# Performance work log

Measured on AMD Instinct MI355X. Metric: run time of the kernel, lower is better.

## Reference

```python
import jax, jax.numpy as jnp
import numpy as np
import math

D_MODEL = 1024
NUM_HEADS = 16
D_KEY = D_MODEL // NUM_HEADS  # 64, used only for the softmax scale
B, S = 4, 2048


def setup_inputs() -> dict:
    key = jax.random.key(0)
    ks = jax.random.split(key, 7)
    scale = 1.0 / math.sqrt(D_MODEL)
    x = jax.random.normal(ks[0], (B, S, D_MODEL), dtype=jnp.float32)
    # torch.nn.Linear params: weight [out, in], bias [out]
    Wq = jax.random.normal(ks[1], (D_MODEL, D_MODEL), dtype=jnp.float32) * scale
    bq = jax.random.normal(ks[2], (D_MODEL,), dtype=jnp.float32) * scale
    Wk = jax.random.normal(ks[3], (D_MODEL, D_MODEL), dtype=jnp.float32) * scale
    bk = jax.random.normal(ks[4], (D_MODEL,), dtype=jnp.float32) * scale
    Wv = jax.random.normal(ks[5], (D_MODEL, D_MODEL), dtype=jnp.float32) * scale
    bv = jax.random.normal(ks[6], (D_MODEL,), dtype=jnp.float32) * scale
    return {"x": x, "Wq": Wq, "bq": bq, "Wk": Wk, "bk": bk, "Wv": Wv, "bv": bv}


def reference(x, Wq, bq, Wk, bk, Wv, bv):
    # Q, K, V projections (torch Linear: x @ W.T + b)
    Q = jnp.einsum('bsd,ed->bse', x, Wq) + bq  # [B,S,D]
    K = jnp.einsum('bsd,ed->bse', x, Wk) + bk
    V = jnp.einsum('bsd,ed->bse', x, Wv) + bv
    inv_sqrt_dk = 1.0 / math.sqrt(D_KEY)
    # full-width attention (no head split, as in the source forward)
    scores = jnp.einsum('bqd,bkd->bqk', Q, K) * inv_sqrt_dk  # [B,S,S]
    weights = jax.nn.softmax(scores, axis=-1)
    return jnp.einsum('bqk,bkd->bqd', weights, V)  # [B,S,D]
```

## Files before the change

kernel.cpp:

```cpp
#include <hip/hip_runtime.h>
#include <stdint.h>

#define S_LEN 2048
#define DMODEL 1024
#define NBATCH 4
#define MROWS (NBATCH * S_LEN)

typedef __bf16 bf16x8 __attribute__((ext_vector_type(8)));
typedef float f32x4 __attribute__((ext_vector_type(4)));

__device__ __forceinline__ unsigned short f2bf(float f) {
  unsigned int x = __builtin_bit_cast(unsigned int, f);
  x += 0x7FFFu + ((x >> 16) & 1u);
  return (unsigned short)(x >> 16);
}

template <int N>
__device__ __forceinline__ void waitvm() {
  static_assert(N <= 8, "vmcnt range");
  if constexpr (N < 0) {}
  else if constexpr (N == 0) asm volatile("s_waitcnt vmcnt(0)" ::: "memory");
  else if constexpr (N == 1) asm volatile("s_waitcnt vmcnt(1)" ::: "memory");
  else if constexpr (N == 2) asm volatile("s_waitcnt vmcnt(2)" ::: "memory");
  else if constexpr (N == 3) asm volatile("s_waitcnt vmcnt(3)" ::: "memory");
  else if constexpr (N == 4) asm volatile("s_waitcnt vmcnt(4)" ::: "memory");
  else if constexpr (N == 5) asm volatile("s_waitcnt vmcnt(5)" ::: "memory");
  else if constexpr (N == 6) asm volatile("s_waitcnt vmcnt(6)" ::: "memory");
  else if constexpr (N == 7) asm volatile("s_waitcnt vmcnt(7)" ::: "memory");
  else asm volatile("s_waitcnt vmcnt(8)" ::: "memory");
}
#define BARRIER() do { __builtin_amdgcn_s_barrier(); asm volatile("" ::: "memory"); } while (0)
#define LGKM0() do { asm volatile("s_waitcnt lgkmcnt(0)" ::: "memory"); \
                     __builtin_amdgcn_sched_barrier(0); } while (0)

__global__ void prep_all_kernel(const float* __restrict__ x, const float* __restrict__ Wq,
                                const float* __restrict__ Wk, const float* __restrict__ Wv,
                                const float* __restrict__ bq, const float* __restrict__ bk,
                                ushort4* __restrict__ xb, ushort4* __restrict__ Wqkb,
                                ushort4* __restrict__ Wvb, float4* __restrict__ bqk) {
  const int NX = MROWS * DMODEL / 4;
  const int NW = DMODEL * DMODEL / 4;
  int i = blockIdx.x * blockDim.x + threadIdx.x;
  float4 v;
  if (i < NX) {
    v = reinterpret_cast<const float4*>(x)[i];
    ushort4 o; o.x = f2bf(v.x); o.y = f2bf(v.y); o.z = f2bf(v.z); o.w = f2bf(v.w);
    xb[i] = o;
  } else {
    int j = i - NX;
    if (j < NW) v = reinterpret_cast<const float4*>(Wq)[j];
    else if (j < 2 * NW) v = reinterpret_cast<const float4*>(Wk)[j - NW];
    else v = reinterpret_cast<const float4*>(Wv)[j - 2 * NW];
    ushort4 o; o.x = f2bf(v.x); o.y = f2bf(v.y); o.z = f2bf(v.z); o.w = f2bf(v.w);
    if (j < 2 * NW) Wqkb[j] = o;
    else Wvb[j - 2 * NW] = o;
    if (j < 512) bqk[j] = (j < 256) ? reinterpret_cast<const float4*>(bq)[j]
                                    : reinterpret_cast<const float4*>(bk)[j - 256];
  }
}

template <int BM_, int EP, int NT>
__global__ __launch_bounds__(512, 2) void gemm8(
    const unsigned short* __restrict__ A, const unsigned short* __restrict__ Bm,
    void* __restrict__ Cp, const float* __restrict__ bias,
    int lda, int ldb, int ldc, float scale,
    long zsA, long zsB, long zsC) {
  constexpr int BN_ = 256;
  constexpr int BK = 64;
  constexpr int RA = BM_ / 128;
  constexpr int HALF_A = (BM_ / 2) * 128;
  constexpr int HALF_B = 128 * 128;
  constexpr int ATILE = BM_ * 128;
  constexpr int BTILE = BN_ * 128;
  constexpr int MREP = BM_ / 32;
  constexpr int MQ = MREP / 2;
  constexpr int VPRO = (BM_ == 256) ? 4 : 3;
  constexpr int W_PA = (BM_ == 256) ? 6 : 4;
  constexpr int W_PB = (BM_ == 256) ? 6 : 5;
  constexpr int W_PC = (BM_ == 256) ? 4 : 3;
  constexpr int VDA  = (BM_ == 256) ? 2 : 1;

  __shared__ alignas(16) char lds[(ATILE + BTILE) * 2];

  const int tid = threadIdx.x;
  const int l = tid & 63;
  const int w = tid >> 6;
  const int wm = w >> 2;
  const int wn = w & 3;

  const int gx = gridDim.x;
  const int nwg = gridDim.x * gridDim.y;
  int n = blockIdx.y * gx + blockIdx.x;
  int n2 = (n & 7) * (nwg >> 3) + (n >> 3);
  const int tileM = (n2 / gx) * BM_;
  const int tileN = (n2 % gx) * BN_;

  const int z = blockIdx.z;
  const unsigned short* Ab = A + (size_t)z * zsA;
  const unsigned short* Bb = Bm + (size_t)z * zsB;

  const int srow = l >> 3;
  const int scol = (((l & 7) ^ srow) * 16);

  auto stageA = [&](int buf, int t, int h) {
#pragma unroll
    for (int r = 0; r < RA; ++r) {
      int row = h * (BM_ / 2) + r * 64 + w * 8 + srow;
      const char* g = (const char*)(Ab + (size_t)(tileM + row) * lda + t * BK) + scol;
      char* d = lds + buf * (ATILE + BTILE) + h * HALF_A + r * 8192 + w * 1024;
      __builtin_amdgcn_global_load_lds(
          (const __attribute__((address_space(1))) void*)g,
          (__attribute__((address_space(3))) void*)d, 16, 0, 0);
    }
  };
  auto stageB = [&](int buf, int t, int h) {
#pragma unroll
    for (int r = 0; r < 2; ++r) {
      int row = h * 128 + r * 64 + w * 8 + srow;
      const char* g = (const char*)(Bb + (size_t)(tileN + row) * ldb + t * BK) + scol;
      char* d = lds + buf * (ATILE + BTILE) + ATILE + h * HALF_B + r * 8192 + w * 1024;
      __builtin_amdgcn_global_load_lds(
          (const __attribute__((address_space(1))) void*)g,
          (__attribute__((address_space(3))) void*)d, 16, 0, 0);
    }
  };

  f32x4 acc[MREP][4];
#pragma unroll
  for (int m = 0; m < MREP; ++m)
#pragma unroll
    for (int nn = 0; nn < 4; ++nn) acc[m][nn] = f32x4{0.f, 0.f, 0.f, 0.f};

  const int frow = l & 15;
  auto rdA = [&](int buf, int mh, int m, int kk) -> bf16x8 {
    int row = mh * (BM_ / 2) + wm * (BM_ / 4) + m * 16 + frow;
    int col = (kk * 64 + ((l >> 4) * 16)) ^ ((row & 7) << 4);
    return *reinterpret_cast<const bf16x8*>(lds + buf * (ATILE + BTILE) + row * 128 + col);
  };
  auto rdB = [&](int buf, int nh, int nn, int kk) -> bf16x8 {
    int row = nh * 128 + wn * 32 + nn * 16 + frow;
    int col = (kk * 64 + ((l >> 4) * 16)) ^ ((row & 7) << 4);
    return *reinterpret_cast<const bf16x8*>(lds + buf * (ATILE + BTILE) + ATILE + row * 128 + col);
  };

  bf16x8 avF[MQ][2];
  bf16x8 bv0[2][2], bv1[2][2];

  auto rdAfull = [&](int buf, int mh) {
#pragma unroll
    for (int m = 0; m < MQ; ++m)
#pragma unroll
      for (int kk = 0; kk < 2; ++kk) avF[m][kk] = rdA(buf, mh, m, kk);
  };
  auto rdBfull = [&](int buf, int nh, bf16x8 (&bv)[2][2]) {
#pragma unroll
    for (int nn = 0; nn < 2; ++nn)
#pragma unroll
      for (int kk = 0; kk < 2; ++kk) bv[nn][kk] = rdB(buf, nh, nn, kk);
  };
  auto mfc = [&](int mh, bf16x8 (&bv)[2][2], int nh) {
    __builtin_amdgcn_s_setprio(1);
#pragma unroll
    for (int kk = 0; kk < 2; ++kk)
#pragma unroll
      for (int m = 0; m < MQ; ++m)
#pragma unroll
        for (int nn = 0; nn < 2; ++nn)
          acc[mh * MQ + m][nh * 2 + nn] = __builtin_amdgcn_mfma_f32_16x16x32_bf16(
              avF[m][kk], bv[nn][kk], acc[mh * MQ + m][nh * 2 + nn], 0, 0, 0);
    __builtin_amdgcn_s_setprio(0);
  };
  auto mfc2 = [&](int mh) {
    __builtin_amdgcn_s_setprio(1);
#pragma unroll
    for (int kk = 0; kk < 2; ++kk)
#pragma unroll
      for (int m = 0; m < MQ; ++m) {
#pragma unroll
        for (int nn = 0; nn < 2; ++nn)
          acc[mh * MQ + m][2 + nn] = __builtin_amdgcn_mfma_f32_16x16x32_bf16(
              avF[m][kk], bv1[nn][kk], acc[mh * MQ + m][2 + nn], 0, 0, 0);
#pragma unroll
        for (int nn = 0; nn < 2; ++nn)
          acc[mh * MQ + m][nn] = __builtin_amdgcn_mfma_f32_16x16x32_bf16(
              avF[m][kk], bv0[nn][kk], acc[mh * MQ + m][nn], 0, 0, 0);
      }
    __builtin_amdgcn_s_setprio(0);
  };

  stageA(0, 0, 0);
  stageB(0, 0, 0);
  stageB(0, 0, 1);
  stageA(0, 0, 1);
  waitvm<VPRO>();
  BARRIER();

#pragma unroll 2
  for (int t = 0; t < NT - 1; ++t) {
    const int buf = t & 1, nb = buf ^ 1;
    rdAfull(buf, 0); rdBfull(buf, 0, bv0);
    stageA(nb, t + 1, 0); stageB(nb, t + 1, 0);
    waitvm<W_PA>(); BARRIER(); LGKM0();
    mfc(0, bv0, 0);
    rdBfull(buf, 1, bv1);
    stageB(nb, t + 1, 1);
    waitvm<W_PB>(); BARRIER(); LGKM0();
    mfc(0, bv1, 1);
    rdAfull(buf, 1);
    stageA(nb, t + 1, 1);
    waitvm<W_PC>(); BARRIER(); LGKM0();
    mfc2(1);
  }
  {
    const int buf = (NT - 1) & 1;
    rdAfull(buf, 0); rdBfull(buf, 0, bv0);
    waitvm<VDA>(); BARRIER(); LGKM0();
    mfc(0, bv0, 0);
    rdBfull(buf, 1, bv1);
    waitvm<0>(); BARRIER(); LGKM0();
    mfc(0, bv1, 1);
    rdAfull(buf, 1);
    LGKM0();
    mfc2(1);
  }

  const int lr = (l >> 4) * 4;
  const int lc = l & 15;
#pragma unroll
  for (int mh = 0; mh < 2; ++mh) {
#pragma unroll
    for (int m = 0; m < MQ; ++m) {
#pragma unroll
      for (int nh = 0; nh < 2; ++nh) {
#pragma unroll
        for (int nn = 0; nn < 2; ++nn) {
          int gr = tileM + mh * (BM_ / 2) + wm * (BM_ / 4) + m * 16 + lr;
          int gc = tileN + nh * 128 + wn * 32 + nn * 16 + lc;
          f32x4 v = acc[mh * MQ + m][nh * 2 + nn];
          if constexpr (EP == 0 || EP == 3) {
            unsigned short* C = (unsigned short*)Cp + (size_t)z * zsC;
#pragma unroll
            for (int j = 0; j < 4; ++j) {
              float bb = (EP == 0) ? bias[gc] : bias[gr + j];
              C[(size_t)(gr + j) * ldc + gc] = f2bf(v[j] + bb);
            }
          } else if constexpr (EP == 4) {
            unsigned short* C = (unsigned short*)Cp + (size_t)z * zsC;
#pragma unroll
            for (int j = 0; j < 4; ++j)
              C[(size_t)(gr + j) * ldc + gc] = f2bf(__expf(v[j] * scale));
          } else if constexpr (EP == 5) {
            float* C = (float*)Cp + (size_t)z * zsC;
#pragma unroll
            for (int j = 0; j < 4; ++j)
              C[(size_t)(gr + j) * ldc + gc] = v[j] * bias[(size_t)z * S_LEN + gr + j];
          } else {
            float* C = (float*)Cp + (size_t)z * zsC;
#pragma unroll
            for (int j = 0; j < 4; ++j)
              C[(size_t)(gr + j) * ldc + gc] = (EP == 1) ? v[j] * scale : v[j];
          }
        }
      }
    }
  }
}

__global__ __launch_bounds__(256) void rowsum_kernel(const unsigned short* __restrict__ P,
                                                     float* __restrict__ rinv) {
  const size_t row = blockIdx.x;
  const ushort4* sp = reinterpret_cast<const ushort4*>(P + row * S_LEN);
  const int t = threadIdx.x;
  const int wid = t >> 6, lane = t & 63;
  ushort4 a = sp[t * 2];
  ushort4 b = sp[t * 2 + 1];
  float s = 0.f;
  s += __builtin_bit_cast(float, (unsigned int)a.x << 16);
  s += __builtin_bit_cast(float, (unsigned int)a.y << 16);
  s += __builtin_bit_cast(float, (unsigned int)a.z << 16);
  s += __builtin_bit_cast(float, (unsigned int)a.w << 16);
  s += __builtin_bit_cast(float, (unsigned int)b.x << 16);
  s += __builtin_bit_cast(float, (unsigned int)b.y << 16);
  s += __builtin_bit_cast(float, (unsigned int)b.z << 16);
  s += __builtin_bit_cast(float, (unsigned int)b.w << 16);
#pragma unroll
  for (int o = 32; o > 0; o >>= 1) s += __shfl_xor(s, o);
  __shared__ float red[4];
  if (lane == 0) red[wid] = s;
  __syncthreads();
  if (t == 0) rinv[row] = 1.0f / (red[0] + red[1] + red[2] + red[3]);
}

extern "C" void kernel_launch(void* const* d_in, const int* in_sizes, int n_in,
                              void* d_out, int out_size, void* d_ws, size_t ws_size,
                              hipStream_t stream) {
  (void)in_sizes; (void)n_in; (void)out_size;
  const float* x = (const float*)d_in[0];
  const float* Wq = (const float*)d_in[1];
  const float* bq = (const float*)d_in[2];
  const float* Wk = (const float*)d_in[3];
  const float* bk = (const float*)d_in[4];
  const float* Wv = (const float*)d_in[5];
  const float* bv = (const float*)d_in[6];
  float* out = (float*)d_out;

  if (ws_size < 108036096ull) return;
  char* ws = (char*)d_ws;
  unsigned short* xb   = (unsigned short*)(ws);
  unsigned short* Wqkb = (unsigned short*)(ws + 16777216);
  unsigned short* Wvb  = (unsigned short*)(ws + 20971520);
  float*          bqk  = (float*)(ws + 23068672);
  unsigned short* QKb  = (unsigned short*)(ws + 24117248);
  unsigned short* P    = (unsigned short*)(ws + 57671680);
  float*          rinv = (float*)(ws + 91226112);
  unsigned short* Vt   = (unsigned short*)(ws + 91258880);

  const int NX = MROWS * DMODEL / 4, NW = DMODEL * DMODEL / 4;
  prep_all_kernel<<<dim3((NX + 3 * NW) / 256), 256, 0, stream>>>(
      x, Wq, Wk, Wv, bq, bk, (ushort4*)xb, (ushort4*)Wqkb, (ushort4*)Wvb, (float4*)bqk);

  gemm8<256, 0, 16><<<dim3(8, 32, 1), 512, 0, stream>>>(
      xb, Wqkb, QKb, bqk, 1024, 1024, 2048, 1.f, 0, 0, 0);

  gemm8<128, 3, 16><<<dim3(8, 8, 4), 512, 0, stream>>>(
      Wvb, xb, Vt, bv, 1024, 1024, 2048, 1.f,
      0, (long)S_LEN * DMODEL, (long)DMODEL * S_LEN);

  gemm8<256, 4, 16><<<dim3(8, 8, 4), 512, 0, stream>>>(
      QKb, QKb + 1024, P, nullptr, 2048, 2048, 2048, 0.125f,
      (long)S_LEN * 2048, (long)S_LEN * 2048, (long)S_LEN * S_LEN);

  rowsum_kernel<<<dim3(MROWS), 256, 0, stream>>>(P, rinv);

  gemm8<128, 5, 32><<<dim3(4, 16, 4), 512, 0, stream>>>(
      P, Vt, out, rinv, 2048, 2048, 1024, 1.f,
      (long)S_LEN * S_LEN, (long)DMODEL * S_LEN, (long)S_LEN * DMODEL);
}
```

Measured before the change: 155.0 us.

## Fuse softmax row-sum into exp GEMM epilogue and drop rowsum kernel

```diff
diff --git a/kernel.cpp b/kernel.cpp
--- a/kernel.cpp
+++ b/kernel.cpp
@@ -13,6 +13,9 @@
   unsigned int x = __builtin_bit_cast(unsigned int, f);
   x += 0x7FFFu + ((x >> 16) & 1u);
   return (unsigned short)(x >> 16);
+}
+__device__ __forceinline__ float bf2f(unsigned short u) {
+  return __builtin_bit_cast(float, (unsigned int)u << 16);
 }
 
 template <int N>
@@ -64,7 +67,7 @@
     const unsigned short* __restrict__ A, const unsigned short* __restrict__ Bm,
     void* __restrict__ Cp, const float* __restrict__ bias,
     int lda, int ldb, int ldc, float scale,
-    long zsA, long zsB, long zsC) {
+    long zsA, long zsB, long zsC, float* __restrict__ rsum) {
   constexpr int BN_ = 256;
   constexpr int BK = 64;
   constexpr int RA = BM_ / 128;
@@ -81,6 +84,7 @@
   constexpr int VDA  = (BM_ == 256) ? 2 : 1;
 
   __shared__ alignas(16) char lds[(ATILE + BTILE) * 2];
+  __shared__ float srinv[(EP == 5) ? 128 : 4];
 
   const int tid = threadIdx.x;
   const int l = tid & 63;
@@ -98,6 +102,17 @@
   const int z = blockIdx.z;
   const unsigned short* Ab = A + (size_t)z * zsA;
   const unsigned short* Bb = Bm + (size_t)z * zsB;
+
+  if constexpr (EP == 5) {
+    if (tid < BM_) {
+      const float* rp = bias + (size_t)z * 32 * S_LEN + (tileM + tid);
+      float s = 0.f;
+#pragma unroll
+      for (int i = 0; i < 32; ++i) s += rp[(size_t)i * S_LEN];
+      srinv[tid] = 1.0f / s;
+    }
+    asm volatile("s_waitcnt lgkmcnt(0)" ::: "memory");
+  }
 
   const int srow = l >> 3;
   const int scol = (((l & 7) ^ srow) * 16);
@@ -226,69 +241,80 @@
 
   const int lr = (l >> 4) * 4;
   const int lc = l & 15;
-#pragma unroll
-  for (int mh = 0; mh < 2; ++mh) {
-#pragma unroll
-    for (int m = 0; m < MQ; ++m) {
-#pragma unroll
-      for (int nh = 0; nh < 2; ++nh) {
-#pragma unroll
-        for (int nn = 0; nn < 2; ++nn) {
-          int gr = tileM + mh * (BM_ / 2) + wm * (BM_ / 4) + m * 16 + lr;
-          int gc = tileN + nh * 128 + wn * 32 + nn * 16 + lc;
-          f32x4 v = acc[mh * MQ + m][nh * 2 + nn];
-          if constexpr (EP == 0 || EP == 3) {
-            unsigned short* C = (unsigned short*)Cp + (size_t)z * zsC;
-#pragma unroll
-            for (int j = 0; j < 4; ++j) {
-              float bb = (EP == 0) ? bias[gc] : bias[gr + j];
-              C[(size_t)(gr + j) * ldc + gc] = f2bf(v[j] + bb);
+  if constexpr (EP == 4) {
+    unsigned short* C = (unsigned short*)Cp + (size_t)z * zsC;
+    const int sidx = (n2 % gx) * 4 + wn;
+#pragma unroll
+    for (int mh = 0; mh < 2; ++mh) {
+#pragma unroll
+      for (int m = 0; m < MQ; ++m) {
+        const int gr0 = tileM + mh * (BM_ / 2) + wm * (BM_ / 4) + m * 16 + lr;
+        float rs0 = 0.f, rs1 = 0.f, rs2 = 0.f, rs3 = 0.f;
+#pragma unroll
+        for (int nh = 0; nh < 2; ++nh) {
+#pragma unroll
+          for (int nn = 0; nn < 2; ++nn) {
+            int gc = tileN + nh * 128 + wn * 32 + nn * 16 + lc;
+            f32x4 v = acc[mh * MQ + m][nh * 2 + nn];
+            unsigned short p0 = f2bf(__expf(v[0] * scale));
+            unsigned short p1 = f2bf(__expf(v[1] * scale));
+            unsigned short p2 = f2bf(__expf(v[2] * scale));
+            unsigned short p3 = f2bf(__expf(v[3] * scale));
+            C[(size_t)(gr0 + 0) * ldc + gc] = p0;
+            C[(size_t)(gr0 + 1) * ldc + gc] = p1;
+            C[(size_t)(gr0 + 2) * ldc + gc] = p2;
+            C[(size_t)(gr0 + 3) * ldc + gc] = p3;
+            rs0 += bf2f(p0); rs1 += bf2f(p1); rs2 += bf2f(p2); rs3 += bf2f(p3);
+          }
+        }
+#pragma unroll
+        for (int off = 1; off < 16; off <<= 1) {
+          rs0 += __shfl_xor(rs0, off);
+          rs1 += __shfl_xor(rs1, off);
+          rs2 += __shfl_xor(rs2, off);
+          rs3 += __shfl_xor(rs3, off);
+        }
+        if ((l & 15) == 0) {
+          float4 rv = {rs0, rs1, rs2, rs3};
+          *reinterpret_cast<float4*>(rsum + ((size_t)z * 32 + sidx) * S_LEN + gr0) = rv;
+        }
+      }
+    }
+  } else {
+#pragma unroll
+    for (int mh = 0; mh < 2; ++mh) {
+#pragma unroll
+      for (int m = 0; m < MQ; ++m) {
+#pragma unroll
+        for (int nh = 0; nh < 2; ++nh) {
+#pragma unroll
+          for (int nn = 0; nn < 2; ++nn) {
+            int gr = tileM + mh * (BM_ / 2) + wm * (BM_ / 4) + m * 16 + lr;
+            int gc = tileN + nh * 128 + wn * 32 + nn * 16 + lc;
+            f32x4 v = acc[mh * MQ + m][nh * 2 + nn];
+            if constexpr (EP == 0 || EP == 3) {
+              unsigned short* C = (unsigned short*)Cp + (size_t)z * zsC;
+#pragma unroll
+              for (int j = 0; j < 4; ++j) {
+                float bb = (EP == 0) ? bias[gc] : bias[gr + j];
+                C[(size_t)(gr + j) * ldc + gc] = f2bf(v[j] + bb);
+              }
+            } else if constexpr (EP == 5) {
+              float* C = (float*)Cp + (size_t)z * zsC;
+#pragma unroll
+              for (int j = 0; j < 4; ++j)
+                C[(size_t)(gr + j) * ldc + gc] = v[j] * srinv[gr - tileM + j];
+            } else {
+              float* C = (float*)Cp + (size_t)z * zsC;
+#pragma unroll
+              for (int j = 0; j < 4; ++j)
+                C[(size_t)(gr + j) * ldc + gc] = (EP == 1) ? v[j] * scale : v[j];
             }
-          } else if constexpr (EP == 4) {
-            unsigned short* C = (unsigned short*)Cp + (size_t)z * zsC;
-#pragma unroll
-            for (int j = 0; j < 4; ++j)
-              C[(size_t)(gr + j) * ldc + gc] = f2bf(__expf(v[j] * scale));
-          } else if constexpr (EP == 5) {
-            float* C = (float*)Cp + (size_t)z * zsC;
-#pragma unroll
-            for (int j = 0; j < 4; ++j)
-              C[(size_t)(gr + j) * ldc + gc] = v[j] * bias[(size_t)z * S_LEN + gr + j];
-          } else {
-            float* C = (float*)Cp + (size_t)z * zsC;
-#pragma unroll
-            for (int j = 0; j < 4; ++j)
-              C[(size_t)(gr + j) * ldc + gc] = (EP == 1) ? v[j] * scale : v[j];
           }
         }
       }
     }
   }
-}
-
-__global__ __launch_bounds__(256) void rowsum_kernel(const unsigned short* __restrict__ P,
-                                                     float* __restrict__ rinv) {
-  const size_t row = blockIdx.x;
-  const ushort4* sp = reinterpret_cast<const ushort4*>(P + row * S_LEN);
-  const int t = threadIdx.x;
-  const int wid = t >> 6, lane = t & 63;
-  ushort4 a = sp[t * 2];
-  ushort4 b = sp[t * 2 + 1];
-  float s = 0.f;
-  s += __builtin_bit_cast(float, (unsigned int)a.x << 16);
-  s += __builtin_bit_cast(float, (unsigned int)a.y << 16);
-  s += __builtin_bit_cast(float, (unsigned int)a.z << 16);
-  s += __builtin_bit_cast(float, (unsigned int)a.w << 16);
-  s += __builtin_bit_cast(float, (unsigned int)b.x << 16);
-  s += __builtin_bit_cast(float, (unsigned int)b.y << 16);
-  s += __builtin_bit_cast(float, (unsigned int)b.z << 16);
-  s += __builtin_bit_cast(float, (unsigned int)b.w << 16);
-#pragma unroll
-  for (int o = 32; o > 0; o >>= 1) s += __shfl_xor(s, o);
-  __shared__ float red[4];
-  if (lane == 0) red[wid] = s;
-  __syncthreads();
-  if (t == 0) rinv[row] = 1.0f / (red[0] + red[1] + red[2] + red[3]);
 }
 
 extern "C" void kernel_launch(void* const* d_in, const int* in_sizes, int n_in,
@@ -304,35 +330,33 @@
   const float* bv = (const float*)d_in[6];
   float* out = (float*)d_out;
 
-  if (ws_size < 108036096ull) return;
+  if (ws_size < 109051904ull) return;
   char* ws = (char*)d_ws;
-  unsigned short* xb   = (unsigned short*)(ws);
-  unsigned short* Wqkb = (unsigned short*)(ws + 16777216);
-  unsigned short* Wvb  = (unsigned short*)(ws + 20971520);
-  float*          bqk  = (float*)(ws + 23068672);
-  unsigned short* QKb  = (unsigned short*)(ws + 24117248);
-  unsigned short* P    = (unsigned short*)(ws + 57671680);
-  float*          rinv = (float*)(ws + 91226112);
-  unsigned short* Vt   = (unsigned short*)(ws + 91258880);
+  unsigned short* xb    = (unsigned short*)(ws);
+  unsigned short* Wqkb  = (unsigned short*)(ws + 16777216);
+  unsigned short* Wvb   = (unsigned short*)(ws + 20971520);
+  float*          bqk   = (float*)(ws + 23068672);
+  unsigned short* QKb   = (unsigned short*)(ws + 24117248);
+  unsigned short* P     = (unsigned short*)(ws + 57671680);
+  float*          rsumP = (float*)(ws + 91226112);
+  unsigned short* Vt    = (unsigned short*)(ws + 92274688);
 
   const int NX = MROWS * DMODEL / 4, NW = DMODEL * DMODEL / 4;
   prep_all_kernel<<<dim3((NX + 3 * NW) / 256), 256, 0, stream>>>(
       x, Wq, Wk, Wv, bq, bk, (ushort4*)xb, (ushort4*)Wqkb, (ushort4*)Wvb, (float4*)bqk);
 
   gemm8<256, 0, 16><<<dim3(8, 32, 1), 512, 0, stream>>>(
-      xb, Wqkb, QKb, bqk, 1024, 1024, 2048, 1.f, 0, 0, 0);
+      xb, Wqkb, QKb, bqk, 1024, 1024, 2048, 1.f, 0, 0, 0, nullptr);
 
   gemm8<128, 3, 16><<<dim3(8, 8, 4), 512, 0, stream>>>(
       Wvb, xb, Vt, bv, 1024, 1024, 2048, 1.f,
-      0, (long)S_LEN * DMODEL, (long)DMODEL * S_LEN);
+      0, (long)S_LEN * DMODEL, (long)DMODEL * S_LEN, nullptr);
 
   gemm8<256, 4, 16><<<dim3(8, 8, 4), 512, 0, stream>>>(
       QKb, QKb + 1024, P, nullptr, 2048, 2048, 2048, 0.125f,
-      (long)S_LEN * 2048, (long)S_LEN * 2048, (long)S_LEN * S_LEN);
-
-  rowsum_kernel<<<dim3(MROWS), 256, 0, stream>>>(P, rinv);
+      (long)S_LEN * 2048, (long)S_LEN * 2048, (long)S_LEN * S_LEN, rsumP);
 
   gemm8<128, 5, 32><<<dim3(4, 16, 4), 512, 0, stream>>>(
-      P, Vt, out, rinv, 2048, 2048, 1024, 1.f,
-      (long)S_LEN * S_LEN, (long)DMODEL * S_LEN, (long)S_LEN * DMODEL);
-}
+      P, Vt, out, rsumP, 2048, 2048, 1024, 1.f,
+      (long)S_LEN * S_LEN, (long)DMODEL * S_LEN, (long)S_LEN * DMODEL, nullptr);
+}
```

Measured after the change: 157.8 us. Within noise of the previous version (+1.8%).
